# Kernel optimization log

Measured on AMD Instinct MI355X. Metric: run time of the kernel, lower is better.

## Reference

```python
import jax, jax.numpy as jnp
import numpy as np

B_SZ, T, N, H = 8, 4096, 256, 512  # batch, seq, num_neurons, d_hidden
RMAX, RMIN = 0.99, 0.4


def _glorot_half(k, shape):
    # VarianceScaling(scale=0.5, mode='fan_avg', distribution='uniform')
    fan_avg = (shape[0] + shape[1]) / 2.0
    limit = float(np.sqrt(3.0 * 0.5 / fan_avg))
    return jax.random.uniform(k, shape, jnp.float32, -limit, limit)


def setup_inputs() -> dict:
    key = jax.random.key(0)
    ks = jax.random.split(key, 8)
    x = jax.random.normal(ks[0], (B_SZ, T, N), jnp.float32)
    C_re = _glorot_half(ks[1], (H, N))
    C_im = _glorot_half(ks[2], (H, N))
    B_re = _glorot_half(ks[3], (N, H))
    B_im = _glorot_half(ks[4], (N, H))
    D = jax.random.normal(ks[5], (N,), jnp.float32)
    numin = float(np.log(-np.log(RMAX)))
    numax = float(np.log(-np.log(RMIN)))
    nu = jax.random.uniform(ks[6], (H,), jnp.float32, numin, numax)
    theta = jax.random.uniform(ks[7], (H,), jnp.float32, 0.0, 3.14 / 10)
    lam_abs = jnp.exp(-jnp.exp(nu))  # |lambda| = |exp(-exp(nu) + i*theta)|
    gamma_log = jnp.log(jnp.sqrt(1.0 - lam_abs ** 2))
    return dict(x=x, B_re=B_re, B_im=B_im, C_re=C_re, C_im=C_im,
                D=D, nu=nu, theta=theta, gamma_log=gamma_log)


def _binary_op(qi, qj):
    A_i, b_i = qi
    A_j, b_j = qj
    return (A_j * A_i, A_j * b_i + b_j)


def reference(x, B_re, B_im, C_re, C_im, D, nu, theta, gamma_log):
    u = x  # adapter is identity since n_in == num_neurons
    lam_log = jax.lax.complex(-jnp.exp(nu), theta)            # (H,) log-lambda
    lam = jnp.exp(lam_log)                                     # (H,) diagonal transition
    gamma = jnp.exp(gamma_log).astype(jnp.complex64)           # (H,)
    Bm = jax.lax.complex(B_re, B_im)                           # (N,H)
    Cm = jax.lax.complex(C_re, C_im)                           # (H,N)
    u_c = u.astype(jnp.complex64)
    bu = gamma * (u_c @ Bm)                                    # (B,T,H) complex64
    A = jnp.broadcast_to(lam, (1, u.shape[1], lam.shape[0]))   # (1,T,H), broadcasts in op
    _, xs = jax.lax.associative_scan(_binary_op, (A, bu), axis=1)  # (B,T,H)
    y = jnp.real(xs @ Cm) + D * u                              # (B,T,N) float32
    return y
```

## Files before the change

### kernel.cpp

```cpp
#include <hip/hip_runtime.h>

#define B_SZ 8
#define T_LEN 4096
#define N_DIM 256
#define H_DIM 512
#define NC 32
#define CL 128
#define ROWS (B_SZ * T_LEN)

#define BM 128
#define BN 128
#define BKg 32

typedef __attribute__((ext_vector_type(4))) float f32x4;
typedef __attribute__((ext_vector_type(8))) short bf16x8;

static __device__ __forceinline__ unsigned short f2bf(float f) {
    unsigned int u = __float_as_uint(f);
    unsigned int r = (u + 0x7FFFu + ((u >> 16) & 1u)) >> 16;
    return (unsigned short)r;
}
static __device__ __forceinline__ float bf2f(unsigned short s) {
    return __uint_as_float(((unsigned int)s) << 16);
}

static __device__ __forceinline__ void lam_of(const float* __restrict__ nu,
                                              const float* __restrict__ theta,
                                              int h, float& lre, float& lim) {
    float r = __expf(-__expf(nu[h]));
    float th = theta[h];
    lre = r * __cosf(th);
    lim = r * __sinf(th);
}

static __device__ __forceinline__ void csum4(const float* __restrict__ nu,
                                             const float* __restrict__ theta,
                                             int h, int pb,
                                             const float* ur, const float* ui,
                                             float& outr, float& outi) {
    const float e  = __expf(nu[h]);
    const float th = theta[h];
    const float p3 = (float)(pb - 48);
    const float r3 = __expf(-p3 * e);
    float w_r = r3 * __cosf(p3 * th);
    float w_i = r3 * __sinf(p3 * th);
    const float r16 = __expf(-16.f * e);
    const float l_r = r16 * __cosf(16.f * th);
    const float l_i = r16 * __sinf(16.f * th);
    float sr = w_r * ur[3] - w_i * ui[3];
    float si = w_r * ui[3] + w_i * ur[3];
#pragma unroll
    for (int m = 2; m >= 0; --m) {
        const float nwr = w_r * l_r - w_i * l_i;
        const float nwi = w_r * l_i + w_i * l_r;
        w_r = nwr; w_i = nwi;
        sr += w_r * ur[m] - w_i * ui[m];
        si += w_r * ui[m] + w_i * ur[m];
    }
    outr = sr; outi = si;
}

__global__ __launch_bounds__(256) void conv_x(const float4* __restrict__ x, ushort4* __restrict__ xb) {
    int id = blockIdx.x * 256 + threadIdx.x;
    float4 v = x[id];
    ushort4 o;
    o.x = f2bf(v.x); o.y = f2bf(v.y); o.z = f2bf(v.z); o.w = f2bf(v.w);
    xb[id] = o;
}

__global__ __launch_bounds__(256) void conv_Bt(const float* __restrict__ Bre,
                                               const float* __restrict__ Bim,
                                               unsigned short* __restrict__ BT1) {
    int id = blockIdx.x * 256 + threadIdx.x;
    int k = id >> 9, h = id & 511;
    BT1[(long)(2 * h) * 256 + k]     = f2bf(Bre[id]);
    BT1[(long)(2 * h + 1) * 256 + k] = f2bf(Bim[id]);
}

__global__ __launch_bounds__(256) void conv_Ct(const float* __restrict__ Cre,
                                               const float* __restrict__ Cim,
                                               unsigned short* __restrict__ CT) {
    int id = blockIdx.x * 256 + threadIdx.x;
    int h = id >> 8, nn = id & 255;
    CT[(long)nn * 1024 + 2 * h]     = f2bf(Cre[id]);
    CT[(long)nn * 1024 + 2 * h + 1] = f2bf(-Cim[id]);
}

template <int MODE>
__global__ __launch_bounds__(256) void gemm_mfma(const unsigned short* __restrict__ A,
                                                 const unsigned short* __restrict__ Bt,
                                                 int M, int N, int K,
                                                 const float* __restrict__ e0,
                                                 const float* __restrict__ e1,
                                                 const unsigned short* __restrict__ e1b,
                                                 const float* __restrict__ nu,
                                                 const float* __restrict__ theta,
                                                 float4* __restrict__ sums,
                                                 void* __restrict__ out) {
    __shared__ __align__(16) unsigned short As[3][BM * BKg];
    __shared__ __align__(16) unsigned short Bs[3][BN * BKg];
    const int tid = threadIdx.x;
    const int lane = tid & 63;
    const int wave = tid >> 6;
    const int wr = wave >> 1, wc = wave & 1;

    const int nwg = (int)gridDim.x;
    const int cpx = nwg >> 3;
    const int bid = (int)blockIdx.x;
    const int tile = (bid & 7) * cpx + (bid >> 3);

    const int nTilesN = N / BN;
    const long tileM = (long)(tile / nTilesN) * BM;
    const long tileN = (long)(tile % nTilesN) * BN;

    const int rsub = lane >> 2;
    const int sg = 8 * ((lane & 3) ^ ((lane >> 3) & 3));
    const unsigned short* Abase = A + tileM * (long)K + sg;
    const unsigned short* Bbase = Bt + tileN * (long)K + sg;

    auto stage = [&](int buf, int k0) {
#pragma unroll
        for (int cc = 0; cc < 2; ++cc) {
            const int c = wave + cc * 4;
            const int row = c * 16 + rsub;
            const unsigned short* ga = Abase + (long)row * K + k0;
            __builtin_amdgcn_global_load_lds((const __attribute__((address_space(1))) unsigned int*)ga,
                                             (__attribute__((address_space(3))) unsigned int*)(As[buf] + c * 512),
                                             16, 0, 0);
            const unsigned short* gb = Bbase + (long)row * K + k0;
            __builtin_amdgcn_global_load_lds((const __attribute__((address_space(1))) unsigned int*)gb,
                                             (__attribute__((address_space(3))) unsigned int*)(Bs[buf] + c * 512),
                                             16, 0, 0);
        }
    };

    const int rdA = 16 * ((lane >> 4) ^ ((lane >> 1) & 3));

    f32x4 acc[4][4] = {};
    const int nt = K / BKg;

    stage(0, 0);
    stage(1, BKg);

    int cur = 0, pf = 2;
    for (int t = 0; t < nt; ++t) {
        if (t + 2 < nt) {
            stage(pf, (t + 2) * BKg);
            asm volatile("s_waitcnt vmcnt(8)" ::: "memory");
        } else if (t + 1 < nt) {
            asm volatile("s_waitcnt vmcnt(4)" ::: "memory");
        } else {
            asm volatile("s_waitcnt vmcnt(0)" ::: "memory");
        }
        __builtin_amdgcn_s_barrier();
        asm volatile("" ::: "memory");

        bf16x8 af[4], bfr[4];
#pragma unroll
        for (int m = 0; m < 4; ++m) {
            const int row = wr * 64 + m * 16 + (lane & 15);
            af[m] = *(const bf16x8*)((const char*)As[cur] + row * 64 + rdA);
        }
#pragma unroll
        for (int n = 0; n < 4; ++n) {
            const int row = wc * 64 + n * 16 + (lane & 15);
            bfr[n] = *(const bf16x8*)((const char*)Bs[cur] + row * 64 + rdA);
        }
#pragma unroll
        for (int m = 0; m < 4; ++m)
#pragma unroll
            for (int n = 0; n < 4; ++n)
                acc[m][n] = __builtin_amdgcn_mfma_f32_16x16x32_bf16(bfr[n], af[m], acc[m][n], 0, 0, 0);

        asm volatile("" ::: "memory");
        __builtin_amdgcn_s_barrier();
        asm volatile("" ::: "memory");

        cur = (cur == 2) ? 0 : cur + 1;
        pf = (pf == 2) ? 0 : pf + 1;
    }

    const int fr = lane & 15;
    const int fs = lane >> 4;
    if constexpr (MODE == 0) {
        unsigned short* o = (unsigned short*)out;
        float s_r0[4], s_i0[4], s_r1[4], s_i1[4];
        const int pb = 127 - wr * 64 - fr;
#pragma unroll
        for (int n = 0; n < 4; ++n) {
            const int col0 = (int)tileN + wc * 64 + n * 16 + fs * 4;
            const int h0 = col0 >> 1;
            const float g0 = __expf(e0[h0]);
            const float g1 = __expf(e0[h0 + 1]);
            float ur0[4], ui0[4], ur1[4], ui1[4];
#pragma unroll
            for (int m = 0; m < 4; ++m) {
                const long grow = tileM + wr * 64 + m * 16 + fr;
                const float v0 = acc[m][n][0] * g0;
                const float v1 = acc[m][n][1] * g0;
                const float v2 = acc[m][n][2] * g1;
                const float v3 = acc[m][n][3] * g1;
                ushort4 pk;
                pk.x = f2bf(v0); pk.y = f2bf(v1); pk.z = f2bf(v2); pk.w = f2bf(v3);
                *(ushort4*)(o + grow * N + col0) = pk;
                ur0[m] = v0; ui0[m] = v1; ur1[m] = v2; ui1[m] = v3;
            }
            csum4(nu, theta, h0,     pb, ur0, ui0, s_r0[n], s_i0[n]);
            csum4(nu, theta, h0 + 1, pb, ur1, ui1, s_r1[n], s_i1[n]);
        }
#pragma unroll
        for (int n = 0; n < 4; ++n) {
#pragma unroll
            for (int st = 1; st < 16; st <<= 1) {
                s_r0[n] += __shfl_xor(s_r0[n], st);
                s_i0[n] += __shfl_xor(s_i0[n], st);
                s_r1[n] += __shfl_xor(s_r1[n], st);
                s_i1[n] += __shfl_xor(s_i1[n], st);
            }
        }
        __syncthreads();
        float4* red = (float4*)As;
        if (fr == 0) {
#pragma unroll
            for (int n = 0; n < 4; ++n)
                red[wr * 32 + wc * 16 + n * 4 + fs] = make_float4(s_r0[n], s_i0[n], s_r1[n], s_i1[n]);
        }
        __syncthreads();
        if (tid < 32) {
            float4 a = red[tid], b2 = red[32 + tid];
            sums[(long)(tileM >> 7) * 256 + (tileN >> 2) + tid] =
                make_float4(a.x + b2.x, a.y + b2.y, a.z + b2.z, a.w + b2.w);
        }
    } else {
        float* o = (float*)out;
#pragma unroll
        for (int n = 0; n < 4; ++n) {
            const int col0 = (int)tileN + wc * 64 + n * 16 + fs * 4;
            const float4 dv = *(const float4*)(e0 + col0);
#pragma unroll
            for (int m = 0; m < 4; ++m) {
                const long grow = tileM + wr * 64 + m * 16 + fr;
                const long idx = grow * N + col0;
                float u0, u1, u2, u3;
                if (e1b) {
                    ushort4 ub = *(const ushort4*)(e1b + idx);
                    u0 = bf2f(ub.x); u1 = bf2f(ub.y); u2 = bf2f(ub.z); u3 = bf2f(ub.w);
                } else {
                    float4 uf = *(const float4*)(e1 + idx);
                    u0 = uf.x; u1 = uf.y; u2 = uf.z; u3 = uf.w;
                }
                float4 st;
                st.x = acc[m][n][0] + dv.x * u0;
                st.y = acc[m][n][1] + dv.y * u1;
                st.z = acc[m][n][2] + dv.z * u2;
                st.w = acc[m][n][3] + dv.w * u3;
                *(float4*)(o + idx) = st;
            }
        }
    }
}


__global__ __launch_bounds__(256) void k2b_carry(const float4* __restrict__ sums,
                                                 float4* __restrict__ carry,
                                                 const float* __restrict__ nu,
                                                 const float* __restrict__ theta) {
    const int gid = blockIdx.x * 256 + threadIdx.x;
    const int hp = gid & 255;
    const int b = gid >> 8;
    float lre0, lim0, lre1, lim1;
    lam_of(nu, theta, 2 * hp, lre0, lim0);
    lam_of(nu, theta, 2 * hp + 1, lre1, lim1);
    float p0r = lre0, p0i = lim0, p1r = lre1, p1i = lim1;
#pragma unroll
    for (int i = 0; i < 7; ++i) {
        float t0 = p0r * p0r - p0i * p0i; p0i = 2.f * p0r * p0i; p0r = t0;
        float t1 = p1r * p1r - p1i * p1i; p1i = 2.f * p1r * p1i; p1r = t1;
    }
    float c0r = 0.f, c0i = 0.f, c1r = 0.f, c1i = 0.f;
#pragma unroll
    for (int c = 0; c < NC; ++c) {
        long idx = ((long)b * NC + c) * 256 + hp;
        carry[idx] = make_float4(c0r, c0i, c1r, c1i);
        float4 s = sums[idx];
        float t0 = fmaf(p0r, c0r, fmaf(-p0i, c0i, s.x));
        c0i = fmaf(p0r, c0i, fmaf(p0i, c0r, s.y));
        c0r = t0;
        float t1 = fmaf(p1r, c1r, fmaf(-p1i, c1i, s.z));
        c1i = fmaf(p1r, c1i, fmaf(p1i, c1r, s.w));
        c1r = t1;
    }
}

__global__ __launch_bounds__(256) void k2ac_scan(ushort4* __restrict__ xs4,
                                                 const float4* __restrict__ carry,
                                                 const float* __restrict__ nu,
                                                 const float* __restrict__ theta) {
    const int gid = blockIdx.x * 256 + threadIdx.x;
    const int hp = gid & 255;
    const int c = (gid >> 8) & (NC - 1);
    const int b = gid >> 13;
    float lre0, lim0, lre1, lim1;
    lam_of(nu, theta, 2 * hp, lre0, lim0);
    lam_of(nu, theta, 2 * hp + 1, lre1, lim1);
    float4 cr = carry[((long)b * NC + c) * 256 + hp];
    float a0r = cr.x, a0i = cr.y, a1r = cr.z, a1i = cr.w;
    long base = ((long)b * T_LEN + (long)c * CL) * 256 + hp;
#pragma unroll 4
    for (int i = 0; i < CL; ++i) {
        ushort4 v = xs4[base + (long)i * 256];
        float u0r = bf2f(v.x), u0i = bf2f(v.y), u1r = bf2f(v.z), u1i = bf2f(v.w);
        float n0r = fmaf(lre0, a0r, fmaf(-lim0, a0i, u0r));
        float n0i = fmaf(lre0, a0i, fmaf(lim0, a0r, u0i));
        float n1r = fmaf(lre1, a1r, fmaf(-lim1, a1i, u1r));
        float n1i = fmaf(lre1, a1i, fmaf(lim1, a1r, u1i));
        a0r = n0r; a0i = n0i; a1r = n1r; a1i = n1i;
        ushort4 o;
        o.x = f2bf(a0r); o.y = f2bf(a0i); o.z = f2bf(a1r); o.w = f2bf(a1i);
        xs4[base + (long)i * 256] = o;
    }
}

extern "C" void kernel_launch(void* const* d_in, const int* in_sizes, int n_in,
                              void* d_out, int out_size, void* d_ws, size_t ws_size,
                              hipStream_t stream) {
    const float* x         = (const float*)d_in[0];
    const float* Bre       = (const float*)d_in[1];
    const float* Bim       = (const float*)d_in[2];
    const float* Cre       = (const float*)d_in[3];
    const float* Cim       = (const float*)d_in[4];
    const float* Dv        = (const float*)d_in[5];
    const float* nu        = (const float*)d_in[6];
    const float* theta     = (const float*)d_in[7];
    const float* gamma_log = (const float*)d_in[8];
    float* y = (float*)d_out;

    const size_t XS_BYTES  = (size_t)ROWS * H_DIM * 4;
    const size_t REG_BYTES = 2u * 1024 * 1024;
    const size_t XB_BYTES  = (size_t)ROWS * N_DIM * 2;
    unsigned short* xs_us = (unsigned short*)d_ws;
    ushort4* xs4   = (ushort4*)d_ws;
    char* regionA  = (char*)d_ws + XS_BYTES;
    char* regionB  = regionA + REG_BYTES;
    unsigned short* BT1 = (unsigned short*)regionA;
    unsigned short* CT  = (unsigned short*)regionA;
    float4*  carry = (float4*)regionB;
    float4*  sums  = (float4*)(regionB + 1024 * 1024);

    const bool xb_in_ws = ws_size >= XS_BYTES + 2 * REG_BYTES + XB_BYTES;
    unsigned short* xb = xb_in_ws ? (unsigned short*)(regionB + REG_BYTES)
                                  : (unsigned short*)d_out;

    conv_x<<<ROWS * N_DIM / 4 / 256, 256, 0, stream>>>((const float4*)x, (ushort4*)xb);
    conv_Bt<<<(N_DIM * H_DIM) / 256, 256, 0, stream>>>(Bre, Bim, BT1);

    gemm_mfma<0><<<(ROWS / BM) * (1024 / BN), 256, 0, stream>>>(
        xb, BT1, ROWS, 1024, 256, gamma_log, nullptr, nullptr, nu, theta, sums, xs_us);

    k2b_carry<<<(B_SZ * 256) / 256, 256, 0, stream>>>(sums, carry, nu, theta);
    k2ac_scan<<<(B_SZ * NC * 256) / 256, 256, 0, stream>>>(xs4, carry, nu, theta);

    conv_Ct<<<(H_DIM * N_DIM) / 256, 256, 0, stream>>>(Cre, Cim, CT);

    gemm_mfma<1><<<(ROWS / BM) * (256 / BN), 256, 0, stream>>>(
        xs_us, CT, ROWS, 256, 1024, Dv, x, xb_in_ws ? xb : nullptr, nullptr, nullptr, nullptr, y);
}
```

Measured before the change: 122.0 us.

## Fuse chunk-local scan into the output GEMM prologue, dropping the separate scan pass

The separate scan kernel, which read and rewrote the bf16 xs buffer in place, is removed. The second GEMM now runs one block per 128-row tile over all 256 outputs. For each 128-wide slice of H it applies the carry-seeded recurrence while loading xs, writes the scanned values into swizzled LDS, and feeds them straight to MFMA. This removes one full read and write of the 64 MB xs buffer. The cost is that the serial 128-step recurrence now runs on only 128 threads per block, with LDS at 64 KB and B fragments read directly from global memory without LDS staging.

```diff
diff --git a/kernel.cpp b/kernel.cpp
--- a/kernel.cpp
+++ b/kernel.cpp
@@ -86,17 +86,14 @@
     CT[(long)nn * 1024 + 2 * h + 1] = f2bf(-Cim[id]);
 }
 
-template <int MODE>
-__global__ __launch_bounds__(256) void gemm_mfma(const unsigned short* __restrict__ A,
-                                                 const unsigned short* __restrict__ Bt,
-                                                 int M, int N, int K,
-                                                 const float* __restrict__ e0,
-                                                 const float* __restrict__ e1,
-                                                 const unsigned short* __restrict__ e1b,
-                                                 const float* __restrict__ nu,
-                                                 const float* __restrict__ theta,
-                                                 float4* __restrict__ sums,
-                                                 void* __restrict__ out) {
+__global__ __launch_bounds__(256) void gemm_k1(const unsigned short* __restrict__ A,
+                                               const unsigned short* __restrict__ Bt,
+                                               int N, int K,
+                                               const float* __restrict__ e0,
+                                               const float* __restrict__ nu,
+                                               const float* __restrict__ theta,
+                                               float4* __restrict__ sums,
+                                               unsigned short* __restrict__ out) {
     __shared__ __align__(16) unsigned short As[3][BM * BKg];
     __shared__ __align__(16) unsigned short Bs[3][BN * BKg];
     const int tid = threadIdx.x;
@@ -182,84 +179,55 @@
 
     const int fr = lane & 15;
     const int fs = lane >> 4;
-    if constexpr (MODE == 0) {
-        unsigned short* o = (unsigned short*)out;
-        float s_r0[4], s_i0[4], s_r1[4], s_i1[4];
-        const int pb = 127 - wr * 64 - fr;
-#pragma unroll
-        for (int n = 0; n < 4; ++n) {
-            const int col0 = (int)tileN + wc * 64 + n * 16 + fs * 4;
-            const int h0 = col0 >> 1;
-            const float g0 = __expf(e0[h0]);
-            const float g1 = __expf(e0[h0 + 1]);
-            float ur0[4], ui0[4], ur1[4], ui1[4];
-#pragma unroll
-            for (int m = 0; m < 4; ++m) {
-                const long grow = tileM + wr * 64 + m * 16 + fr;
-                const float v0 = acc[m][n][0] * g0;
-                const float v1 = acc[m][n][1] * g0;
-                const float v2 = acc[m][n][2] * g1;
-                const float v3 = acc[m][n][3] * g1;
-                ushort4 pk;
-                pk.x = f2bf(v0); pk.y = f2bf(v1); pk.z = f2bf(v2); pk.w = f2bf(v3);
-                *(ushort4*)(o + grow * N + col0) = pk;
-                ur0[m] = v0; ui0[m] = v1; ur1[m] = v2; ui1[m] = v3;
-            }
-            csum4(nu, theta, h0,     pb, ur0, ui0, s_r0[n], s_i0[n]);
-            csum4(nu, theta, h0 + 1, pb, ur1, ui1, s_r1[n], s_i1[n]);
-        }
-#pragma unroll
-        for (int n = 0; n < 4; ++n) {
-#pragma unroll
-            for (int st = 1; st < 16; st <<= 1) {
-                s_r0[n] += __shfl_xor(s_r0[n], st);
-                s_i0[n] += __shfl_xor(s_i0[n], st);
-                s_r1[n] += __shfl_xor(s_r1[n], st);
-                s_i1[n] += __shfl_xor(s_i1[n], st);
-            }
-        }
-        __syncthreads();
-        float4* red = (float4*)As;
-        if (fr == 0) {
-#pragma unroll
-            for (int n = 0; n < 4; ++n)
-                red[wr * 32 + wc * 16 + n * 4 + fs] = make_float4(s_r0[n], s_i0[n], s_r1[n], s_i1[n]);
-        }
-        __syncthreads();
-        if (tid < 32) {
-            float4 a = red[tid], b2 = red[32 + tid];
-            sums[(long)(tileM >> 7) * 256 + (tileN >> 2) + tid] =
-                make_float4(a.x + b2.x, a.y + b2.y, a.z + b2.z, a.w + b2.w);
-        }
-    } else {
-        float* o = (float*)out;
-#pragma unroll
-        for (int n = 0; n < 4; ++n) {
-            const int col0 = (int)tileN + wc * 64 + n * 16 + fs * 4;
-            const float4 dv = *(const float4*)(e0 + col0);
-#pragma unroll
-            for (int m = 0; m < 4; ++m) {
-                const long grow = tileM + wr * 64 + m * 16 + fr;
-                const long idx = grow * N + col0;
-                float u0, u1, u2, u3;
-                if (e1b) {
-                    ushort4 ub = *(const ushort4*)(e1b + idx);
-                    u0 = bf2f(ub.x); u1 = bf2f(ub.y); u2 = bf2f(ub.z); u3 = bf2f(ub.w);
-                } else {
-                    float4 uf = *(const float4*)(e1 + idx);
-                    u0 = uf.x; u1 = uf.y; u2 = uf.z; u3 = uf.w;
-                }
-                float4 st;
-                st.x = acc[m][n][0] + dv.x * u0;
-                st.y = acc[m][n][1] + dv.y * u1;
-                st.z = acc[m][n][2] + dv.z * u2;
-                st.w = acc[m][n][3] + dv.w * u3;
-                *(float4*)(o + idx) = st;
-            }
-        }
-    }
-}
-
+    unsigned short* o = out;
+    float s_r0[4], s_i0[4], s_r1[4], s_i1[4];
+    const int pb = 127 - wr * 64 - fr;
+#pragma unroll
+    for (int n = 0; n < 4; ++n) {
+        const int col0 = (int)tileN + wc * 64 + n * 16 + fs * 4;
+        const int h0 = col0 >> 1;
+        const float g0 = __expf(e0[h0]);
+        const float g1 = __expf(e0[h0 + 1]);
+        float ur0[4], ui0[4], ur1[4], ui1[4];
+#pragma unroll
+        for (int m = 0; m < 4; ++m) {
+            const long grow = tileM + wr * 64 + m * 16 + fr;
+            const float v0 = acc[m][n][0] * g0;
+            const float v1 = acc[m][n][1] * g0;
+            const float v2 = acc[m][n][2] * g1;
+            const float v3 = acc[m][n][3] * g1;
+            ushort4 pk;
+            pk.x = f2bf(v0); pk.y = f2bf(v1); pk.z = f2bf(v2); pk.w = f2bf(v3);
+            *(ushort4*)(o + grow * N + col0) = pk;
+            ur0[m] = v0; ui0[m] = v1; ur1[m] = v2; ui1[m] = v3;
+        }
+        csum4(nu, theta, h0,     pb, ur0, ui0, s_r0[n], s_i0[n]);
+        csum4(nu, theta, h0 + 1, pb, ur1, ui1, s_r1[n], s_i1[n]);
+    }
+#pragma unroll
+    for (int n = 0; n < 4; ++n) {
+#pragma unroll
+        for (int st = 1; st < 16; st <<= 1) {
+            s_r0[n] += __shfl_xor(s_r0[n], st);
+            s_i0[n] += __shfl_xor(s_i0[n], st);
+            s_r1[n] += __shfl_xor(s_r1[n], st);
+            s_i1[n] += __shfl_xor(s_i1[n], st);
+        }
+    }
+    __syncthreads();
+    float4* red = (float4*)As;
+    if (fr == 0) {
+#pragma unroll
+        for (int n = 0; n < 4; ++n)
+            red[wr * 32 + wc * 16 + n * 4 + fs] = make_float4(s_r0[n], s_i0[n], s_r1[n], s_i1[n]);
+    }
+    __syncthreads();
+    if (tid < 32) {
+        float4 a = red[tid], b2 = red[32 + tid];
+        sums[(long)(tileM >> 7) * 256 + (tileN >> 2) + tid] =
+            make_float4(a.x + b2.x, a.y + b2.y, a.z + b2.z, a.w + b2.w);
+    }
+}
 
 __global__ __launch_bounds__(256) void k2b_carry(const float4* __restrict__ sums,
                                                  float4* __restrict__ carry,
@@ -292,32 +260,104 @@
     }
 }
 
-__global__ __launch_bounds__(256) void k2ac_scan(ushort4* __restrict__ xs4,
-                                                 const float4* __restrict__ carry,
-                                                 const float* __restrict__ nu,
-                                                 const float* __restrict__ theta) {
-    const int gid = blockIdx.x * 256 + threadIdx.x;
-    const int hp = gid & 255;
-    const int c = (gid >> 8) & (NC - 1);
-    const int b = gid >> 13;
-    float lre0, lim0, lre1, lim1;
-    lam_of(nu, theta, 2 * hp, lre0, lim0);
-    lam_of(nu, theta, 2 * hp + 1, lre1, lim1);
-    float4 cr = carry[((long)b * NC + c) * 256 + hp];
-    float a0r = cr.x, a0i = cr.y, a1r = cr.z, a1i = cr.w;
-    long base = ((long)b * T_LEN + (long)c * CL) * 256 + hp;
-#pragma unroll 4
-    for (int i = 0; i < CL; ++i) {
-        ushort4 v = xs4[base + (long)i * 256];
-        float u0r = bf2f(v.x), u0i = bf2f(v.y), u1r = bf2f(v.z), u1i = bf2f(v.w);
-        float n0r = fmaf(lre0, a0r, fmaf(-lim0, a0i, u0r));
-        float n0i = fmaf(lre0, a0i, fmaf(lim0, a0r, u0i));
-        float n1r = fmaf(lre1, a1r, fmaf(-lim1, a1i, u1r));
-        float n1i = fmaf(lre1, a1i, fmaf(lim1, a1r, u1i));
-        a0r = n0r; a0i = n0i; a1r = n1r; a1i = n1i;
-        ushort4 o;
-        o.x = f2bf(a0r); o.y = f2bf(a0i); o.z = f2bf(a1r); o.w = f2bf(a1i);
-        xs4[base + (long)i * 256] = o;
+__global__ __launch_bounds__(512, 4) void gemm_scan(const unsigned short* __restrict__ xs,
+                                                    const unsigned short* __restrict__ Ct,
+                                                    const float4* __restrict__ carry,
+                                                    const float* __restrict__ Dv,
+                                                    const float* __restrict__ xf,
+                                                    const unsigned short* __restrict__ xb,
+                                                    const float* __restrict__ nu,
+                                                    const float* __restrict__ theta,
+                                                    float* __restrict__ y) {
+    __shared__ __align__(16) unsigned short Asc[128 * 256];
+    const int tid = threadIdx.x;
+    const int lane = tid & 63;
+    const int wave = tid >> 6;
+    const int wr = wave >> 2;
+    const int wc = wave & 3;
+
+    const int nwg = (int)gridDim.x;
+    const int cpx = nwg >> 3;
+    const int bid = (int)blockIdx.x;
+    const int tile = (bid & 7) * cpx + (bid >> 3);
+    const long tileM = (long)tile * 128;
+
+    const int fr = lane & 15;
+    const int fs = lane >> 4;
+
+    f32x4 acc[4][4] = {};
+
+    for (int sc = 0; sc < 4; ++sc) {
+        if (sc) __syncthreads();
+        if (tid < 128) {
+            const int h = sc * 128 + tid;
+            float lre, lim;
+            lam_of(nu, theta, h, lre, lim);
+            const float2 c2 = ((const float2*)carry)[((long)tile * 256 + (h >> 1)) * 2 + (h & 1)];
+            float ar = c2.x, ai = c2.y;
+            const unsigned short* src = xs + tileM * 1024 + 2 * h;
+            char* dst = (char*)Asc + 4 * tid;
+#pragma unroll 8
+            for (int r = 0; r < 128; ++r) {
+                ushort2 v = *(const ushort2*)(src + (long)r * 1024);
+                float ur = bf2f(v.x), ui = bf2f(v.y);
+                float nr = fmaf(lre, ar, fmaf(-lim, ai, ur));
+                float ni = fmaf(lre, ai, fmaf(lim, ar, ui));
+                ar = nr; ai = ni;
+                ushort2 o2;
+                o2.x = f2bf(ar); o2.y = f2bf(ai);
+                *(ushort2*)((char*)Asc + r * 512 + ((4 * tid) ^ ((r & 7) << 4))) = o2;
+            }
+            (void)dst;
+        }
+        __syncthreads();
+
+#pragma unroll
+        for (int kc = 0; kc < 8; ++kc) {
+            bf16x8 af[4], bfr[4];
+#pragma unroll
+            for (int m = 0; m < 4; ++m) {
+                const int row = wr * 64 + m * 16 + fr;
+                af[m] = *(const bf16x8*)((const char*)Asc + row * 512 +
+                                         ((kc * 64 + fs * 16) ^ ((row & 7) << 4)));
+            }
+            const long kush = (long)sc * 256 + kc * 32 + fs * 8;
+#pragma unroll
+            for (int n = 0; n < 4; ++n) {
+                const int col = wc * 64 + n * 16 + fr;
+                bfr[n] = *(const bf16x8*)(Ct + (long)col * 1024 + kush);
+            }
+#pragma unroll
+            for (int m = 0; m < 4; ++m)
+#pragma unroll
+                for (int n = 0; n < 4; ++n)
+                    acc[m][n] = __builtin_amdgcn_mfma_f32_16x16x32_bf16(bfr[n], af[m], acc[m][n], 0, 0, 0);
+        }
+    }
+
+#pragma unroll
+    for (int n = 0; n < 4; ++n) {
+        const int col0 = wc * 64 + n * 16 + fs * 4;
+        const float4 dv = *(const float4*)(Dv + col0);
+#pragma unroll
+        for (int m = 0; m < 4; ++m) {
+            const long grow = tileM + wr * 64 + m * 16 + fr;
+            const long idx = grow * 256 + col0;
+            float u0, u1, u2, u3;
+            if (xb) {
+                ushort4 ub = *(const ushort4*)(xb + idx);
+                u0 = bf2f(ub.x); u1 = bf2f(ub.y); u2 = bf2f(ub.z); u3 = bf2f(ub.w);
+            } else {
+                float4 uf = *(const float4*)(xf + idx);
+                u0 = uf.x; u1 = uf.y; u2 = uf.z; u3 = uf.w;
+            }
+            float4 st;
+            st.x = acc[m][n][0] + dv.x * u0;
+            st.y = acc[m][n][1] + dv.y * u1;
+            st.z = acc[m][n][2] + dv.z * u2;
+            st.w = acc[m][n][3] + dv.w * u3;
+            *(float4*)(y + idx) = st;
+        }
     }
 }
 
@@ -339,7 +379,6 @@
     const size_t REG_BYTES = 2u * 1024 * 1024;
     const size_t XB_BYTES  = (size_t)ROWS * N_DIM * 2;
     unsigned short* xs_us = (unsigned short*)d_ws;
-    ushort4* xs4   = (ushort4*)d_ws;
     char* regionA  = (char*)d_ws + XS_BYTES;
     char* regionB  = regionA + REG_BYTES;
     unsigned short* BT1 = (unsigned short*)regionA;
@@ -354,14 +393,13 @@
     conv_x<<<ROWS * N_DIM / 4 / 256, 256, 0, stream>>>((const float4*)x, (ushort4*)xb);
     conv_Bt<<<(N_DIM * H_DIM) / 256, 256, 0, stream>>>(Bre, Bim, BT1);
 
-    gemm_mfma<0><<<(ROWS / BM) * (1024 / BN), 256, 0, stream>>>(
-        xb, BT1, ROWS, 1024, 256, gamma_log, nullptr, nullptr, nu, theta, sums, xs_us);
+    gemm_k1<<<(ROWS / BM) * (1024 / BN), 256, 0, stream>>>(
+        xb, BT1, 1024, 256, gamma_log, nu, theta, sums, xs_us);
 
     k2b_carry<<<(B_SZ * 256) / 256, 256, 0, stream>>>(sums, carry, nu, theta);
-    k2ac_scan<<<(B_SZ * NC * 256) / 256, 256, 0, stream>>>(xs4, carry, nu, theta);
 
     conv_Ct<<<(H_DIM * N_DIM) / 256, 256, 0, stream>>>(Cre, Cim, CT);
 
-    gemm_mfma<1><<<(ROWS / BM) * (256 / BN), 256, 0, stream>>>(
-        xs_us, CT, ROWS, 256, 1024, Dv, x, xb_in_ws ? xb : nullptr, nullptr, nullptr, nullptr, y);
-}
+    gemm_scan<<<ROWS / 128, 512, 0, stream>>>(
+        xs_us, CT, carry, Dv, x, xb_in_ws ? xb : nullptr, nu, theta, y);
+}
```

Result: slower. 239.4 us (+96.3%).

## Add dedicated first GEMM kernel with full-K B tile resident in LDS

Applied to the files above, without the earlier changes.

Replaces the generic pipelined GEMM used for the input projection with a specialized kernel that loads the entire 128x256 B tile into LDS once, via direct global-to-LDS loads with an XOR swizzle. A fragments are read straight from global memory with no LDS staging, and the K loop (K=256) is fully unrolled with no per-step barriers. The fused epilogue (gamma scaling, bf16 store, chunk sums for the scan) is moved into this kernel and removed from the template. The cost is 64KB of LDS per block, which may limit occupancy, and A reads from global without LDS reuse across waves.

```diff
diff --git a/kernel.cpp b/kernel.cpp
--- a/kernel.cpp
+++ b/kernel.cpp
@@ -86,6 +86,115 @@
     CT[(long)nn * 1024 + 2 * h + 1] = f2bf(-Cim[id]);
 }
 
+__global__ __launch_bounds__(256) void gemm_k1b(const unsigned short* __restrict__ A,
+                                                const unsigned short* __restrict__ Bt,
+                                                const float* __restrict__ e0,
+                                                const float* __restrict__ nu,
+                                                const float* __restrict__ theta,
+                                                float4* __restrict__ sums,
+                                                unsigned short* __restrict__ out) {
+    __shared__ __align__(16) unsigned short Bs[128 * 256];
+    const int tid = threadIdx.x;
+    const int lane = tid & 63;
+    const int wave = tid >> 6;
+    const int wr = wave >> 1, wc = wave & 1;
+
+    const int nwg = (int)gridDim.x;
+    const int cpx = nwg >> 3;
+    const int bid = (int)blockIdx.x;
+    const int tile = (bid & 7) * cpx + (bid >> 3);
+    const long tileM = (long)(tile >> 3) * BM;
+    const long tileN = (long)(tile & 7) * BN;
+
+    const int l5 = lane >> 5;
+    const int s_lin = lane & 31;
+#pragma unroll
+    for (int i = 0; i < 16; ++i) {
+        const int u = wave * 16 + i;
+        const int row = 2 * u + l5;
+        const int sg = 8 * (s_lin ^ ((row & 7) << 2));
+        const unsigned short* gb = Bt + (tileN + row) * 256L + sg;
+        __builtin_amdgcn_global_load_lds((const __attribute__((address_space(1))) unsigned int*)gb,
+                                         (__attribute__((address_space(3))) unsigned int*)(Bs + u * 512),
+                                         16, 0, 0);
+    }
+    __syncthreads();
+
+    const int fr = lane & 15;
+    const int fs = lane >> 4;
+    const int bxr = (fr & 7) << 2;
+
+    f32x4 acc[4][4] = {};
+    const unsigned short* Ab = A + (tileM + wr * 64 + fr) * 256L + fs * 8;
+
+#pragma unroll
+    for (int kc = 0; kc < 8; ++kc) {
+        bf16x8 af[4], bfr[4];
+#pragma unroll
+        for (int m = 0; m < 4; ++m)
+            af[m] = *(const bf16x8*)(Ab + (long)m * 16 * 256 + kc * 32);
+#pragma unroll
+        for (int n = 0; n < 4; ++n) {
+            const int row = wc * 64 + n * 16 + fr;
+            bfr[n] = *(const bf16x8*)((const char*)Bs + row * 512 + 16 * ((kc * 4 + fs) ^ bxr));
+        }
+#pragma unroll
+        for (int m = 0; m < 4; ++m)
+#pragma unroll
+            for (int n = 0; n < 4; ++n)
+                acc[m][n] = __builtin_amdgcn_mfma_f32_16x16x32_bf16(bfr[n], af[m], acc[m][n], 0, 0, 0);
+    }
+
+    unsigned short* o = out;
+    float s_r0[4], s_i0[4], s_r1[4], s_i1[4];
+    const int pb = 127 - wr * 64 - fr;
+#pragma unroll
+    for (int n = 0; n < 4; ++n) {
+        const int col0 = (int)tileN + wc * 64 + n * 16 + fs * 4;
+        const int h0 = col0 >> 1;
+        const float g0 = __expf(e0[h0]);
+        const float g1 = __expf(e0[h0 + 1]);
+        float ur0[4], ui0[4], ur1[4], ui1[4];
+#pragma unroll
+        for (int m = 0; m < 4; ++m) {
+            const long grow = tileM + wr * 64 + m * 16 + fr;
+            const float v0 = acc[m][n][0] * g0;
+            const float v1 = acc[m][n][1] * g0;
+            const float v2 = acc[m][n][2] * g1;
+            const float v3 = acc[m][n][3] * g1;
+            ushort4 pk;
+            pk.x = f2bf(v0); pk.y = f2bf(v1); pk.z = f2bf(v2); pk.w = f2bf(v3);
+            *(ushort4*)(o + grow * 1024 + col0) = pk;
+            ur0[m] = v0; ui0[m] = v1; ur1[m] = v2; ui1[m] = v3;
+        }
+        csum4(nu, theta, h0,     pb, ur0, ui0, s_r0[n], s_i0[n]);
+        csum4(nu, theta, h0 + 1, pb, ur1, ui1, s_r1[n], s_i1[n]);
+    }
+#pragma unroll
+    for (int n = 0; n < 4; ++n) {
+#pragma unroll
+        for (int st = 1; st < 16; st <<= 1) {
+            s_r0[n] += __shfl_xor(s_r0[n], st);
+            s_i0[n] += __shfl_xor(s_i0[n], st);
+            s_r1[n] += __shfl_xor(s_r1[n], st);
+            s_i1[n] += __shfl_xor(s_i1[n], st);
+        }
+    }
+    __syncthreads();
+    float4* red = (float4*)Bs;
+    if (fr == 0) {
+#pragma unroll
+        for (int n = 0; n < 4; ++n)
+            red[wr * 32 + wc * 16 + n * 4 + fs] = make_float4(s_r0[n], s_i0[n], s_r1[n], s_i1[n]);
+    }
+    __syncthreads();
+    if (tid < 32) {
+        float4 a = red[tid], b2 = red[32 + tid];
+        sums[(long)(tileM >> 7) * 256 + (tileN >> 2) + tid] =
+            make_float4(a.x + b2.x, a.y + b2.y, a.z + b2.z, a.w + b2.w);
+    }
+}
+
 template <int MODE>
 __global__ __launch_bounds__(256) void gemm_mfma(const unsigned short* __restrict__ A,
                                                  const unsigned short* __restrict__ Bt,
@@ -93,9 +202,6 @@
                                                  const float* __restrict__ e0,
                                                  const float* __restrict__ e1,
                                                  const unsigned short* __restrict__ e1b,
-                                                 const float* __restrict__ nu,
-                                                 const float* __restrict__ theta,
-                                                 float4* __restrict__ sums,
                                                  void* __restrict__ out) {
     __shared__ __align__(16) unsigned short As[3][BM * BKg];
     __shared__ __align__(16) unsigned short Bs[3][BN * BKg];
@@ -182,56 +288,7 @@
 
     const int fr = lane & 15;
     const int fs = lane >> 4;
-    if constexpr (MODE == 0) {
-        unsigned short* o = (unsigned short*)out;
-        float s_r0[4], s_i0[4], s_r1[4], s_i1[4];
-        const int pb = 127 - wr * 64 - fr;
-#pragma unroll
-        for (int n = 0; n < 4; ++n) {
-            const int col0 = (int)tileN + wc * 64 + n * 16 + fs * 4;
-            const int h0 = col0 >> 1;
-            const float g0 = __expf(e0[h0]);
-            const float g1 = __expf(e0[h0 + 1]);
-            float ur0[4], ui0[4], ur1[4], ui1[4];
-#pragma unroll
-            for (int m = 0; m < 4; ++m) {
-                const long grow = tileM + wr * 64 + m * 16 + fr;
-                const float v0 = acc[m][n][0] * g0;
-                const float v1 = acc[m][n][1] * g0;
-                const float v2 = acc[m][n][2] * g1;
-                const float v3 = acc[m][n][3] * g1;
-                ushort4 pk;
-                pk.x = f2bf(v0); pk.y = f2bf(v1); pk.z = f2bf(v2); pk.w = f2bf(v3);
-                *(ushort4*)(o + grow * N + col0) = pk;
-                ur0[m] = v0; ui0[m] = v1; ur1[m] = v2; ui1[m] = v3;
-            }
-            csum4(nu, theta, h0,     pb, ur0, ui0, s_r0[n], s_i0[n]);
-            csum4(nu, theta, h0 + 1, pb, ur1, ui1, s_r1[n], s_i1[n]);
-        }
-#pragma unroll
-        for (int n = 0; n < 4; ++n) {
-#pragma unroll
-            for (int st = 1; st < 16; st <<= 1) {
-                s_r0[n] += __shfl_xor(s_r0[n], st);
-                s_i0[n] += __shfl_xor(s_i0[n], st);
-                s_r1[n] += __shfl_xor(s_r1[n], st);
-                s_i1[n] += __shfl_xor(s_i1[n], st);
-            }
-        }
-        __syncthreads();
-        float4* red = (float4*)As;
-        if (fr == 0) {
-#pragma unroll
-            for (int n = 0; n < 4; ++n)
-                red[wr * 32 + wc * 16 + n * 4 + fs] = make_float4(s_r0[n], s_i0[n], s_r1[n], s_i1[n]);
-        }
-        __syncthreads();
-        if (tid < 32) {
-            float4 a = red[tid], b2 = red[32 + tid];
-            sums[(long)(tileM >> 7) * 256 + (tileN >> 2) + tid] =
-                make_float4(a.x + b2.x, a.y + b2.y, a.z + b2.z, a.w + b2.w);
-        }
-    } else {
+    {
         float* o = (float*)out;
 #pragma unroll
         for (int n = 0; n < 4; ++n) {
@@ -354,8 +411,8 @@
     conv_x<<<ROWS * N_DIM / 4 / 256, 256, 0, stream>>>((const float4*)x, (ushort4*)xb);
     conv_Bt<<<(N_DIM * H_DIM) / 256, 256, 0, stream>>>(Bre, Bim, BT1);
 
-    gemm_mfma<0><<<(ROWS / BM) * (1024 / BN), 256, 0, stream>>>(
-        xb, BT1, ROWS, 1024, 256, gamma_log, nullptr, nullptr, nu, theta, sums, xs_us);
+    gemm_k1b<<<(ROWS / BM) * (1024 / BN), 256, 0, stream>>>(
+        xb, BT1, gamma_log, nu, theta, sums, xs_us);
 
     k2b_carry<<<(B_SZ * 256) / 256, 256, 0, stream>>>(sums, carry, nu, theta);
     k2ac_scan<<<(B_SZ * NC * 256) / 256, 256, 0, stream>>>(xs4, carry, nu, theta);
@@ -363,5 +420,5 @@
     conv_Ct<<<(H_DIM * N_DIM) / 256, 256, 0, stream>>>(Cre, Cim, CT);
 
     gemm_mfma<1><<<(ROWS / BM) * (256 / BN), 256, 0, stream>>>(
-        xs_us, CT, ROWS, 256, 1024, Dv, x, xb_in_ws ? xb : nullptr, nullptr, nullptr, nullptr, y);
-}
+        xs_us, CT, ROWS, 256, 1024, Dv, x, xb_in_ws ? xb : nullptr, y);
+}
```

Result: slower. 132.2 us (+8.4%).
